# Performance work log

Hardware: AMD Instinct MI355X
Metric: run time of the kernel (lower is better)

The kernel has to match this reference:

```python
import jax, jax.numpy as jnp
import numpy as np

NHEADS = 16
HEAD_DIM = 64
HIDDEN = 1024
QKV = NHEADS * HEAD_DIM  # 1024
SCALING = HEAD_DIM ** -0.5


def setup_inputs() -> dict:
    key = jax.random.key(0)
    k1, k2, k3, k4, k5 = jax.random.split(key, 5)
    B, S = 2, 2048
    hidden_states = jax.random.normal(k1, (B, S, HIDDEN), dtype=jnp.float32)
    # nn.Linear weights: stored [out, in]; kaiming-uniform-ish init scale
    w_qkv = jax.random.normal(k2, (3 * QKV, HIDDEN), dtype=jnp.float32) * (HIDDEN ** -0.5)
    b_qkv = jax.random.normal(k3, (3 * QKV,), dtype=jnp.float32) * 0.01
    w_o = jax.random.normal(k4, (HIDDEN, QKV), dtype=jnp.float32) * (QKV ** -0.5)
    b_o = jax.random.normal(k5, (HIDDEN,), dtype=jnp.float32) * 0.01
    return {"hidden_states": hidden_states, "w_qkv": w_qkv, "b_qkv": b_qkv,
            "w_o": w_o, "b_o": b_o}


def reference(hidden_states, w_qkv, b_qkv, w_o, b_o):
    B, S, _ = hidden_states.shape
    # qkv projection: x @ W^T + b  (torch nn.Linear convention)
    qkv = jnp.einsum('bsh,oh->bso', hidden_states, w_qkv) + b_qkv  # [B,S,3*QKV]
    xq, xk, xv = jnp.split(qkv, 3, axis=-1)
    # [B,S,H,D] -> [B,H,S,D]
    q = xq.reshape(B, S, NHEADS, HEAD_DIM).transpose(0, 2, 1, 3)
    k = xk.reshape(B, S, NHEADS, HEAD_DIM).transpose(0, 2, 1, 3)
    v = xv.reshape(B, S, NHEADS, HEAD_DIM).transpose(0, 2, 1, 3)
    scores = jnp.einsum('bhqd,bhkd->bhqk', q, k) * SCALING
    # dropout is identity in eval mode; mask is None in this config
    probs = jax.nn.softmax(scores.astype(jnp.float32), axis=-1).astype(q.dtype)
    out = jnp.einsum('bhqk,bhkd->bhqd', probs, v)  # [B,H,S,D]
    out = out.transpose(0, 2, 1, 3).reshape(B, S, QKV)
    return jnp.einsum('bsq,oq->bso', out, w_o) + b_o
```

## Files before the change

### kernel.cpp

```cpp
#include <hip/hip_runtime.h>

#define SEQ     2048
#define MROWS   4096
#define HID     1024
#define QKV3    3072
#define NH      16
#define HD      64
#define QSCALE  0.18033688f

typedef unsigned short u16;
typedef unsigned int   u32;
typedef __attribute__((ext_vector_type(8)))  short  bf16x8;
typedef __attribute__((ext_vector_type(4)))  float  floatx4;
typedef __attribute__((ext_vector_type(16))) float  floatx16;
typedef __attribute__((ext_vector_type(4)))  unsigned int u32x4;

__device__ __forceinline__ u16 f2bf(float f) {
    u32 u = __builtin_bit_cast(u32, f);
    u += 0x7fffu + ((u >> 16) & 1u);
    return (u16)(u >> 16);
}

#if __has_builtin(__builtin_amdgcn_exp2f)
__device__ __forceinline__ float fast_exp2(float x) { return __builtin_amdgcn_exp2f(x); }
#else
__device__ __forceinline__ float fast_exp2(float x) { return exp2f(x); }
#endif

#if __has_builtin(__builtin_amdgcn_cvt_pk_bf16_f32)
__device__ __forceinline__ u32 pack_bf(float a, float b) {
    auto r = __builtin_amdgcn_cvt_pk_bf16_f32(a, b);
    return __builtin_bit_cast(u32, r);
}
#else
__device__ __forceinline__ u32 pack_bf(float a, float b) {
    u32 ua = __builtin_bit_cast(u32, a) + 0x8000u;
    u32 ub = __builtin_bit_cast(u32, b) + 0x8000u;
    return __builtin_amdgcn_perm(ub, ua, 0x07060302u);
}
#endif

__device__ __forceinline__ void plane_swap(u32 &x, u32 &y) {
#if __has_builtin(__builtin_amdgcn_permlane32_swap)
    typedef __attribute__((ext_vector_type(2))) unsigned int u32x2;
    u32x2 r = __builtin_amdgcn_permlane32_swap(x, y, false, false);
    x = r[0]; y = r[1];
#else
    asm volatile("v_permlane32_swap_b32 %0, %1" : "+v"(x), "+v"(y));
#endif
}

__device__ __forceinline__ void async_cp16(const void* g, void* l) {
    __builtin_amdgcn_global_load_lds(
        (const __attribute__((address_space(1))) unsigned int*)g,
        (__attribute__((address_space(3))) unsigned int*)l, 16, 0, 0);
}

#define N4_X   (MROWS * HID / 4)
#define N4_WQ  (QKV3 * HID / 4)
#define N4_WO  (HID * HID / 4)
__global__ void cvt_all(const float* __restrict__ x, const float* __restrict__ wq,
                        const float* __restrict__ wo, u16* __restrict__ xb,
                        u16* __restrict__ wqb, u16* __restrict__ wob) {
    int i = blockIdx.x * blockDim.x + threadIdx.x;
    const float* src; u16* dst; int k;
    if (i < N4_X)                { src = x;  dst = xb;  k = i; }
    else if (i < N4_X + N4_WQ)   { src = wq; dst = wqb; k = i - N4_X; }
    else                         { src = wo; dst = wob; k = i - N4_X - N4_WQ; }
    float4 v = ((const float4*)src)[k];
    uint2 o = {pack_bf(v.x, v.y), pack_bf(v.z, v.w)};
    ((uint2*)dst)[k] = o;
}

template <int MODE, int NT>
__global__ __launch_bounds__(256)
void gemm_bf16_nt(const u16* __restrict__ A, const u16* __restrict__ B,
                  const float* __restrict__ bias, float* __restrict__ Cout,
                  int M, int N, int K,
                  u16* __restrict__ q_ws, u16* __restrict__ k_ws,
                  u16* __restrict__ vt_ws) {
    constexpr int WN = NT / 2;
    constexpr int NJ = WN / 16;
    __shared__ u16 As[2][128 * 32];
    __shared__ u16 Bs[2][NT * 32];
    const int t  = (int)threadIdx.x;
    const int w  = t >> 6, l = t & 63;
    const int wr = w >> 1, wc = w & 1;
    const int m0 = (int)blockIdx.y * 128, n0 = (int)blockIdx.x * NT;
    const int lrow = l >> 2;
    const int lseg = ((l & 3) ^ ((l >> 3) & 3)) * 8;
    const int fm = l & 15, fq = l >> 4;
    const int fseg = (fq ^ ((fm >> 1) & 3)) * 8;

    auto stage = [&](int k0, int bb) {
#pragma unroll
        for (int rep = 0; rep < 2; ++rep) {
            const int chunk = w + rep * 4;
            const int row   = chunk * 16 + lrow;
            async_cp16(A + (size_t)(m0 + row) * K + k0 + lseg, &As[bb][chunk * 512]);
            if (NT == 128 || rep == 0)
                async_cp16(B + (size_t)(n0 + row) * K + k0 + lseg, &Bs[bb][chunk * 512]);
        }
    };

    floatx4 acc[4][NJ];
#pragma unroll
    for (int i = 0; i < 4; ++i)
#pragma unroll
        for (int j = 0; j < NJ; ++j) acc[i][j] = (floatx4)(0.f);

    const int T = K >> 5;
    stage(0, 0);
    for (int tt = 0; tt < T; ++tt) {
        const int cur = tt & 1;
        __syncthreads();
        if (tt + 1 < T) stage((tt + 1) << 5, cur ^ 1);
        bf16x8 af[4], bfr[NJ];
#pragma unroll
        for (int i = 0; i < 4; ++i)
            af[i] = *(const bf16x8*)&As[cur][(wr * 64 + i * 16 + fm) * 32 + fseg];
#pragma unroll
        for (int j = 0; j < NJ; ++j)
            bfr[j] = *(const bf16x8*)&Bs[cur][(wc * WN + j * 16 + fm) * 32 + fseg];
#pragma unroll
        for (int i = 0; i < 4; ++i)
#pragma unroll
            for (int j = 0; j < NJ; ++j)
                acc[i][j] = __builtin_amdgcn_mfma_f32_16x16x32_bf16(
                    af[i], bfr[j], acc[i][j], 0, 0, 0);
    }

#pragma unroll
    for (int j = 0; j < NJ; ++j) {
        const int col = n0 + wc * WN + j * 16 + fm;
        const float bv = bias[col];
        const int region = col >> 10;
        const int hh = (col >> 6) & 15, d = col & 63;
#pragma unroll
        for (int i = 0; i < 4; ++i) {
            const int row0 = m0 + wr * 64 + i * 16 + fq * 4;
            if (MODE == 0) {
#pragma unroll
                for (int r = 0; r < 4; ++r)
                    Cout[(size_t)(row0 + r) * N + col] = acc[i][j][r] + bv;
            } else if (region < 2) {
                u16* __restrict__ dst = (region == 0) ? q_ws : k_ws;
                const float sc = (region == 0) ? QSCALE : 1.0f;
#pragma unroll
                for (int r = 0; r < 4; ++r) {
                    const int row = row0 + r;
                    const int b = row >> 11, s = row & 2047;
                    dst[((size_t)(b * NH + hh) * SEQ + s) * HD + d] =
                        f2bf((acc[i][j][r] + bv) * sc);
                }
            } else {
                const int b = row0 >> 11, s0 = row0 & 2047;
                uint2 o = {pack_bf(acc[i][j][0] + bv, acc[i][j][1] + bv),
                           pack_bf(acc[i][j][2] + bv, acc[i][j][3] + bv)};
                *(uint2*)&vt_ws[((size_t)(b * NH + hh) * HD + d) * SEQ + s0] = o;
            }
        }
    }
}

__global__ __launch_bounds__(256, 2)
void attn_mfma(const u16* __restrict__ qw, const u16* __restrict__ kw,
               const u16* __restrict__ vtw, u16* __restrict__ attn) {
    __shared__ u16 Ks [2][2][64 * 64];
    __shared__ u16 Vts[2][2][64 * 64];

    const int bh   = (int)blockIdx.x;
    const int qblk = (int)blockIdx.y * 128;
    const int t = (int)threadIdx.x;
    const int w = t >> 6, l = t & 63;
    const int ql = l & 31, h = l >> 5;
    const int srow = l >> 3, sseg = l & 7;
    const size_t headSD = (size_t)bh * SEQ * HD;
    const size_t headDS = (size_t)bh * HD * SEQ;

    auto stage = [&](int it, int bb) {
#pragma unroll
        for (int half = 0; half < 2; ++half) {
            const int kt = it * 2 + half;
#pragma unroll
            for (int rep = 0; rep < 2; ++rep) {
                const int chunk = w * 2 + rep;
                async_cp16(kw + headSD + (size_t)(kt * 64 + chunk * 8 + srow) * HD
                               + ((sseg ^ srow) * 8), &Ks[bb][half][chunk * 512]);
                async_cp16(vtw + headDS + (size_t)(chunk * 8 + srow) * SEQ + kt * 64
                               + ((sseg ^ srow) * 8), &Vts[bb][half][chunk * 512]);
            }
        }
    };

    bf16x8 qa[4];
#pragma unroll
    for (int ks = 0; ks < 4; ++ks)
        qa[ks] = *(const bf16x8*)(qw + headSD
            + (size_t)(qblk + w * 32 + ql) * HD + ks * 16 + h * 8);

    const floatx16 z16 = (floatx16)(0.f);
    floatx16 oacc[2];
    oacc[0] = z16; oacc[1] = z16;
    float2 psum2 = {0.f, 0.f};

    stage(0, 0);
    for (int it = 0; it < SEQ / 128; ++it) {
        const int cur = it & 1;
        __syncthreads();
        if (it + 1 < SEQ / 128) stage(it + 1, cur ^ 1);

        floatx16 sacc[2][2];
#pragma unroll
        for (int half = 0; half < 2; ++half) {
#pragma unroll
            for (int ks = 0; ks < 4; ++ks) {
                const int seg = ((ks * 2 + h) ^ (ql & 7)) * 8;
#pragma unroll
                for (int t2 = 0; t2 < 2; ++t2) {
                    bf16x8 ka = *(const bf16x8*)&Ks[cur][half][(t2 * 32 + ql) * 64 + seg];
                    sacc[half][t2] = __builtin_amdgcn_mfma_f32_32x32x16_bf16(
                        ka, qa[ks], (ks == 0) ? z16 : sacc[half][t2], 0, 0, 0);
                }
            }
        }

#pragma unroll
        for (int half = 0; half < 2; ++half) {
#pragma unroll
            for (int t2 = 0; t2 < 2; ++t2) {
                u32 aw[8];
#pragma unroll
                for (int i = 0; i < 8; ++i) {
                    const float p0 = fast_exp2(sacc[half][t2][2 * i]);
                    const float p1 = fast_exp2(sacc[half][t2][2 * i + 1]);
                    psum2 += float2{p0, p1};
                    aw[i] = pack_bf(p0, p1);
                }
                plane_swap(aw[0], aw[2]); plane_swap(aw[1], aw[3]);
                plane_swap(aw[4], aw[6]); plane_swap(aw[5], aw[7]);

#pragma unroll
                for (int ks2 = 0; ks2 < 2; ++ks2) {
                    u32x4 pw = {aw[4 * ks2 + 0], aw[4 * ks2 + 1],
                                aw[4 * ks2 + 2], aw[4 * ks2 + 3]};
                    bf16x8 pb = __builtin_bit_cast(bf16x8, pw);
                    const int seg = ((t2 * 4 + ks2 * 2 + h) ^ (ql & 7)) * 8;
#pragma unroll
                    for (int dt = 0; dt < 2; ++dt) {
                        bf16x8 va = *(const bf16x8*)&Vts[cur][half][(dt * 32 + ql) * 64 + seg];
                        oacc[dt] = __builtin_amdgcn_mfma_f32_32x32x16_bf16(
                            va, pb, oacc[dt], 0, 0, 0);
                    }
                }
            }
        }
    }

    float psum = psum2.x + psum2.y;
    psum += __shfl_xor(psum, 32);
    const float inv = 1.0f / psum;

    const int b = bh >> 4, head = bh & 15;
    u16* __restrict__ orow =
        attn + (size_t)(b * SEQ + qblk + w * 32 + ql) * HID + head * HD;
#pragma unroll
    for (int dt = 0; dt < 2; ++dt) {
#pragma unroll
        for (int g = 0; g < 4; ++g) {
            uint2 o = {pack_bf(oacc[dt][g * 4 + 0] * inv, oacc[dt][g * 4 + 1] * inv),
                       pack_bf(oacc[dt][g * 4 + 2] * inv, oacc[dt][g * 4 + 3] * inv)};
            *(uint2*)&orow[dt * 32 + g * 8 + h * 4] = o;
        }
    }
}

extern "C" void kernel_launch(void* const* d_in, const int* in_sizes, int n_in,
                              void* d_out, int out_size, void* d_ws, size_t ws_size,
                              hipStream_t stream) {
    const float* x     = (const float*)d_in[0];
    const float* w_qkv = (const float*)d_in[1];
    const float* b_qkv = (const float*)d_in[2];
    const float* w_o   = (const float*)d_in[3];
    const float* b_o   = (const float*)d_in[4];
    float* outp = (float*)d_out;

    u16* xb    = (u16*)d_ws;
    u16* wqkvb = xb    + (size_t)MROWS * HID;
    u16* wob   = wqkvb + (size_t)QKV3 * HID;
    u16* q_ws  = wob   + (size_t)HID * HID;
    u16* k_ws  = q_ws  + (size_t)MROWS * HID;
    u16* vt_ws = k_ws  + (size_t)MROWS * HID;
    u16* attnb = vt_ws + (size_t)MROWS * HID;

    const int blk = 256;
    cvt_all<<<(N4_X + N4_WQ + N4_WO) / blk, blk, 0, stream>>>(
        x, w_qkv, w_o, xb, wqkvb, wob);

    gemm_bf16_nt<1, 128><<<dim3(QKV3 / 128, MROWS / 128), blk, 0, stream>>>(
        xb, wqkvb, b_qkv, nullptr, MROWS, QKV3, HID, q_ws, k_ws, vt_ws);

    attn_mfma<<<dim3(NH * 2, SEQ / 128), 256, 0, stream>>>(q_ws, k_ws, vt_ws, attnb);

    gemm_bf16_nt<0, 64><<<dim3(HID / 64, MROWS / 128), blk, 0, stream>>>(
        attnb, wob, b_o, outp, MROWS, HID, HID, nullptr, nullptr, nullptr);
}
```

Baseline: 183.3 us.

## Split attention KV tiles across waves with shared-memory reduction of partial outputs

The attention kernel now gives each block 64 queries instead of 128, doubling the grid. Each of the four waves handles a distinct 32-key sub-tile for both 32-query tiles, and each K/V LDS fragment load feeds two MFMAs. Partial outputs and row sums are then reduced across waves through shared memory before normalization and a vectorized store. This raises block count and operand reuse per LDS load, at the cost of twice the K/V global traffic per query and an extra LDS reduction epilogue.

```diff
diff --git a/kernel.cpp b/kernel.cpp
--- a/kernel.cpp
+++ b/kernel.cpp
@@ -166,13 +166,15 @@
 __global__ __launch_bounds__(256, 2)
 void attn_mfma(const u16* __restrict__ qw, const u16* __restrict__ kw,
                const u16* __restrict__ vtw, u16* __restrict__ attn) {
-    __shared__ u16 Ks [2][2][64 * 64];
-    __shared__ u16 Vts[2][2][64 * 64];
+    __shared__ __align__(16) u16 Ks [2][2][64 * 64];
+    __shared__ __align__(16) u16 Vts[2][2][64 * 64];
+    __shared__ float psr[256];
 
     const int bh   = (int)blockIdx.x;
-    const int qblk = (int)blockIdx.y * 128;
+    const int qblk = (int)blockIdx.y * 64;
     const int t = (int)threadIdx.x;
     const int w = t >> 6, l = t & 63;
+    const int whalf = w >> 1, wt2 = w & 1;
     const int ql = l & 31, h = l >> 5;
     const int srow = l >> 3, sseg = l & 7;
     const size_t headSD = (size_t)bh * SEQ * HD;
@@ -193,16 +195,18 @@
         }
     };
 
-    bf16x8 qa[4];
-#pragma unroll
-    for (int ks = 0; ks < 4; ++ks)
-        qa[ks] = *(const bf16x8*)(qw + headSD
-            + (size_t)(qblk + w * 32 + ql) * HD + ks * 16 + h * 8);
+    bf16x8 qa[2][4];
+#pragma unroll
+    for (int qt = 0; qt < 2; ++qt)
+#pragma unroll
+        for (int ks = 0; ks < 4; ++ks)
+            qa[qt][ks] = *(const bf16x8*)(qw + headSD
+                + (size_t)(qblk + qt * 32 + ql) * HD + ks * 16 + h * 8);
 
     const floatx16 z16 = (floatx16)(0.f);
-    floatx16 oacc[2];
-    oacc[0] = z16; oacc[1] = z16;
-    float2 psum2 = {0.f, 0.f};
+    floatx16 oacc[2][2];
+    oacc[0][0] = z16; oacc[0][1] = z16; oacc[1][0] = z16; oacc[1][1] = z16;
+    float2 ps2[2] = {{0.f, 0.f}, {0.f, 0.f}};
 
     stage(0, 0);
     for (int it = 0; it < SEQ / 128; ++it) {
@@ -210,69 +214,97 @@
         __syncthreads();
         if (it + 1 < SEQ / 128) stage(it + 1, cur ^ 1);
 
-        floatx16 sacc[2][2];
-#pragma unroll
-        for (int half = 0; half < 2; ++half) {
-#pragma unroll
-            for (int ks = 0; ks < 4; ++ks) {
-                const int seg = ((ks * 2 + h) ^ (ql & 7)) * 8;
-#pragma unroll
-                for (int t2 = 0; t2 < 2; ++t2) {
-                    bf16x8 ka = *(const bf16x8*)&Ks[cur][half][(t2 * 32 + ql) * 64 + seg];
-                    sacc[half][t2] = __builtin_amdgcn_mfma_f32_32x32x16_bf16(
-                        ka, qa[ks], (ks == 0) ? z16 : sacc[half][t2], 0, 0, 0);
+        floatx16 sacc[2];
+#pragma unroll
+        for (int ks = 0; ks < 4; ++ks) {
+            const int seg = ((ks * 2 + h) ^ (ql & 7)) * 8;
+            bf16x8 ka = *(const bf16x8*)&Ks[cur][whalf][(wt2 * 32 + ql) * 64 + seg];
+            sacc[0] = __builtin_amdgcn_mfma_f32_32x32x16_bf16(
+                ka, qa[0][ks], (ks == 0) ? z16 : sacc[0], 0, 0, 0);
+            sacc[1] = __builtin_amdgcn_mfma_f32_32x32x16_bf16(
+                ka, qa[1][ks], (ks == 0) ? z16 : sacc[1], 0, 0, 0);
+        }
+
+        u32 aw[2][8];
+#pragma unroll
+        for (int qt = 0; qt < 2; ++qt) {
+#pragma unroll
+            for (int i = 0; i < 8; ++i) {
+                const float p0 = fast_exp2(sacc[qt][2 * i]);
+                const float p1 = fast_exp2(sacc[qt][2 * i + 1]);
+                ps2[qt] += float2{p0, p1};
+                aw[qt][i] = pack_bf(p0, p1);
+            }
+            plane_swap(aw[qt][0], aw[qt][2]); plane_swap(aw[qt][1], aw[qt][3]);
+            plane_swap(aw[qt][4], aw[qt][6]); plane_swap(aw[qt][5], aw[qt][7]);
+        }
+
+#pragma unroll
+        for (int ks2 = 0; ks2 < 2; ++ks2) {
+            const int seg = ((wt2 * 4 + ks2 * 2 + h) ^ (ql & 7)) * 8;
+            bf16x8 pb0 = __builtin_bit_cast(bf16x8,
+                (u32x4){aw[0][4*ks2+0], aw[0][4*ks2+1], aw[0][4*ks2+2], aw[0][4*ks2+3]});
+            bf16x8 pb1 = __builtin_bit_cast(bf16x8,
+                (u32x4){aw[1][4*ks2+0], aw[1][4*ks2+1], aw[1][4*ks2+2], aw[1][4*ks2+3]});
+#pragma unroll
+            for (int dt = 0; dt < 2; ++dt) {
+                bf16x8 va = *(const bf16x8*)&Vts[cur][whalf][(dt * 32 + ql) * 64 + seg];
+                oacc[dt][0] = __builtin_amdgcn_mfma_f32_32x32x16_bf16(
+                    va, pb0, oacc[dt][0], 0, 0, 0);
+                oacc[dt][1] = __builtin_amdgcn_mfma_f32_32x32x16_bf16(
+                    va, pb1, oacc[dt][1], 0, 0, 0);
+            }
+        }
+    }
+
+    __syncthreads();
+    float* redK = (float*)&Ks[0][0][0];
+    float* redV = (float*)&Vts[0][0][0];
+    {
+        float* redw = (w < 2) ? redK : redV;
+        const int wloc = w & 1;
+#pragma unroll
+        for (int dt = 0; dt < 2; ++dt)
+#pragma unroll
+            for (int qt = 0; qt < 2; ++qt)
+#pragma unroll
+                for (int g = 0; g < 4; ++g) {
+                    float4 v = {oacc[dt][qt][4*g+0], oacc[dt][qt][4*g+1],
+                                oacc[dt][qt][4*g+2], oacc[dt][qt][4*g+3]};
+                    *(float4*)&redw[((wloc * 64) + qt * 32 + ql) * 64
+                                    + dt * 32 + g * 8 + h * 4] = v;
                 }
-            }
-        }
-
-#pragma unroll
-        for (int half = 0; half < 2; ++half) {
-#pragma unroll
-            for (int t2 = 0; t2 < 2; ++t2) {
-                u32 aw[8];
-#pragma unroll
-                for (int i = 0; i < 8; ++i) {
-                    const float p0 = fast_exp2(sacc[half][t2][2 * i]);
-                    const float p1 = fast_exp2(sacc[half][t2][2 * i + 1]);
-                    psum2 += float2{p0, p1};
-                    aw[i] = pack_bf(p0, p1);
-                }
-                plane_swap(aw[0], aw[2]); plane_swap(aw[1], aw[3]);
-                plane_swap(aw[4], aw[6]); plane_swap(aw[5], aw[7]);
-
-#pragma unroll
-                for (int ks2 = 0; ks2 < 2; ++ks2) {
-                    u32x4 pw = {aw[4 * ks2 + 0], aw[4 * ks2 + 1],
-                                aw[4 * ks2 + 2], aw[4 * ks2 + 3]};
-                    bf16x8 pb = __builtin_bit_cast(bf16x8, pw);
-                    const int seg = ((t2 * 4 + ks2 * 2 + h) ^ (ql & 7)) * 8;
-#pragma unroll
-                    for (int dt = 0; dt < 2; ++dt) {
-                        bf16x8 va = *(const bf16x8*)&Vts[cur][half][(dt * 32 + ql) * 64 + seg];
-                        oacc[dt] = __builtin_amdgcn_mfma_f32_32x32x16_bf16(
-                            va, pb, oacc[dt], 0, 0, 0);
-                    }
-                }
-            }
-        }
     }
-
-    float psum = psum2.x + psum2.y;
-    psum += __shfl_xor(psum, 32);
-    const float inv = 1.0f / psum;
-
+    float ps0 = ps2[0].x + ps2[0].y; ps0 += __shfl_xor(ps0, 32);
+    float ps1 = ps2[1].x + ps2[1].y; ps1 += __shfl_xor(ps1, 32);
+    if (h == 0) { psr[w * 64 + ql] = ps0; psr[w * 64 + 32 + ql] = ps1; }
+    __syncthreads();
+
+    const int q = t >> 2, dq = (t & 3) * 16;
+    float a16[16];
+#pragma unroll
+    for (int i = 0; i < 16; ++i) a16[i] = 0.f;
+#pragma unroll
+    for (int wv = 0; wv < 2; ++wv)
+#pragma unroll
+        for (int i = 0; i < 4; ++i) {
+            float4 v0 = *(const float4*)&redK[(wv * 64 + q) * 64 + dq + i * 4];
+            float4 v1 = *(const float4*)&redV[(wv * 64 + q) * 64 + dq + i * 4];
+            a16[i*4+0] += v0.x + v1.x; a16[i*4+1] += v0.y + v1.y;
+            a16[i*4+2] += v0.z + v1.z; a16[i*4+3] += v0.w + v1.w;
+        }
+    const float pst = psr[q] + psr[64 + q] + psr[128 + q] + psr[192 + q];
+    const float inv = 1.0f / pst;
     const int b = bh >> 4, head = bh & 15;
     u16* __restrict__ orow =
-        attn + (size_t)(b * SEQ + qblk + w * 32 + ql) * HID + head * HD;
-#pragma unroll
-    for (int dt = 0; dt < 2; ++dt) {
-#pragma unroll
-        for (int g = 0; g < 4; ++g) {
-            uint2 o = {pack_bf(oacc[dt][g * 4 + 0] * inv, oacc[dt][g * 4 + 1] * inv),
-                       pack_bf(oacc[dt][g * 4 + 2] * inv, oacc[dt][g * 4 + 3] * inv)};
-            *(uint2*)&orow[dt * 32 + g * 8 + h * 4] = o;
-        }
-    }
+        attn + (size_t)(b * SEQ + qblk + q) * HID + head * HD + dq;
+    u32 ow[8];
+#pragma unroll
+    for (int i = 0; i < 8; ++i) ow[i] = pack_bf(a16[2*i] * inv, a16[2*i+1] * inv);
+    uint4 o0 = {ow[0], ow[1], ow[2], ow[3]};
+    uint4 o1 = {ow[4], ow[5], ow[6], ow[7]};
+    *(uint4*)&orow[0] = o0;
+    *(uint4*)&orow[8] = o1;
 }
 
 extern "C" void kernel_launch(void* const* d_in, const int* in_sizes, int n_in,
@@ -300,7 +332,7 @@
     gemm_bf16_nt<1, 128><<<dim3(QKV3 / 128, MROWS / 128), blk, 0, stream>>>(
         xb, wqkvb, b_qkv, nullptr, MROWS, QKV3, HID, q_ws, k_ws, vt_ws);
 
-    attn_mfma<<<dim3(NH * 2, SEQ / 128), 256, 0, stream>>>(q_ws, k_ws, vt_ws, attnb);
+    attn_mfma<<<dim3(NH * 2, SEQ / 64), 256, 0, stream>>>(q_ws, k_ws, vt_ws, attnb);
 
     gemm_bf16_nt<0, 64><<<dim3(HID / 64, MROWS / 128), blk, 0, stream>>>(
         attnb, wob, b_o, outp, MROWS, HID, HID, nullptr, nullptr, nullptr);
```

New measurement: 195.2 us. 1.06x slower.
